# Kernel optimization log

Measured on AMD Instinct MI355X. Metric: run time of the kernel, lower is better.

## Reference

```python
import jax, jax.numpy as jnp
import numpy as np

NUM_STEPS = 5
RELAX = 1.5
EPS = 1e-5
SIZE = 128
OUT = 128
HSIZE = SIZE + OUT  # feature transformer width (256)


def bn_inf(x, g, b, m, v):
    # inference batch norm with running stats
    return g * (x - m) * jax.lax.rsqrt(v + EPS) + b


def glu(h):
    return h[:, :HSIZE] * jax.nn.sigmoid(h[:, HSIZE:])


def sparsemax(z):
    d = z.shape[-1]
    z_sorted = -jnp.sort(-z, axis=-1)  # descending
    z_cum = jnp.cumsum(z_sorted, axis=-1)
    k = jnp.arange(1, d + 1, dtype=z.dtype)
    support = 1.0 + k * z_sorted > z_cum
    k_z = jnp.sum(support, axis=-1, keepdims=True)  # int support size
    tau = (jnp.take_along_axis(z_cum, k_z - 1, axis=-1) - 1.0) / k_z.astype(z.dtype)
    return jnp.maximum(z - tau, 0.0)


def feat_transformer(x, Ws0, Ws1, Wu_t, g, b, m, v):
    # 4 GLU FeatureBlocks: blocks 0,1 use shared fc weights, 2,3 unshared
    sqrt_half = jnp.sqrt(jnp.asarray(0.5, x.dtype))
    h = glu(bn_inf(x @ Ws0, g[0], b[0], m[0], v[0]))
    h = h * sqrt_half + glu(bn_inf(h @ Ws1, g[1], b[1], m[1], v[1]))
    h = h * sqrt_half + glu(bn_inf(h @ Wu_t[0], g[2], b[2], m[2], v[2]))
    h = h * sqrt_half + glu(bn_inf(h @ Wu_t[1], g[3], b[3], m[3], v[3]))
    return h


def setup_inputs() -> dict:
    key = jax.random.key(0)
    ks = jax.random.split(key, 20)
    B, F = 32768, 512
    U = 2 * HSIZE  # GLU fc units = 512
    T = NUM_STEPS + 1
    sc = 0.05
    inp = {}
    inp['features'] = jax.random.normal(ks[0], (B, F), jnp.float32)
    inp['bn0_g'] = 1.0 + 0.1 * jax.random.normal(ks[1], (F,), jnp.float32)
    inp['bn0_b'] = 0.1 * jax.random.normal(ks[2], (F,), jnp.float32)
    inp['bn0_m'] = 0.1 * jax.random.normal(ks[3], (F,), jnp.float32)
    inp['bn0_v'] = jax.random.uniform(ks[4], (F,), jnp.float32, 0.5, 1.5)
    inp['Ws0'] = sc * jax.random.normal(ks[5], (F, U), jnp.float32)
    inp['Ws1'] = sc * jax.random.normal(ks[6], (HSIZE, U), jnp.float32)
    inp['Wu'] = sc * jax.random.normal(ks[7], (T, 2, HSIZE, U), jnp.float32)
    inp['ft_g'] = 1.0 + 0.1 * jax.random.normal(ks[8], (T, 4, U), jnp.float32)
    inp['ft_b'] = 0.1 * jax.random.normal(ks[9], (T, 4, U), jnp.float32)
    inp['ft_m'] = 0.1 * jax.random.normal(ks[10], (T, 4, U), jnp.float32)
    inp['ft_v'] = jax.random.uniform(ks[11], (T, 4, U), jnp.float32, 0.5, 1.5)
    inp['W_att'] = sc * jax.random.normal(ks[12], (NUM_STEPS, SIZE, F), jnp.float32)
    inp['att_g'] = 1.0 + 0.1 * jax.random.normal(ks[13], (NUM_STEPS, F), jnp.float32)
    inp['att_b'] = 0.1 * jax.random.normal(ks[14], (NUM_STEPS, F), jnp.float32)
    inp['att_m'] = 0.1 * jax.random.normal(ks[15], (NUM_STEPS, F), jnp.float32)
    inp['att_v'] = jax.random.uniform(ks[16], (NUM_STEPS, F), jnp.float32, 0.5, 1.5)
    inp['Wf'] = sc * jax.random.normal(ks[17], (SIZE, OUT), jnp.float32)
    inp['bf'] = jnp.zeros((OUT,), jnp.float32)
    return inp


def reference(features, bn0_g, bn0_b, bn0_m, bn0_v, Ws0, Ws1, Wu,
              ft_g, ft_b, ft_m, ft_v, W_att, att_g, att_b, att_m, att_v, Wf, bf):
    B = features.shape[0]
    feats = bn_inf(features, bn0_g, bn0_b, bn0_m, bn0_v)
    prior = jnp.ones_like(feats)
    out_acc = jnp.zeros((B, OUT), feats.dtype)
    x = feat_transformer(feats, Ws0, Ws1, Wu[0], ft_g[0], ft_b[0], ft_m[0], ft_v[0])
    masks = []
    for s in range(NUM_STEPS):
        att = bn_inf(x[:, OUT:] @ W_att[s], att_g[s], att_b[s], att_m[s], att_v[s])
        mask = sparsemax(att * prior)
        prior = prior * (RELAX - mask)
        masks.append(mask)
        x = feat_transformer(mask * feats, Ws0, Ws1, Wu[s + 1],
                             ft_g[s + 1], ft_b[s + 1], ft_m[s + 1], ft_v[s + 1])
        out_acc = out_acc + jax.nn.relu(x[:, :OUT])
    final = out_acc @ Wf + bf
    return final, jnp.stack(masks)
```

## Files before the change

### kernel.cpp

```cpp
#include <hip/hip_runtime.h>
#include <hip/hip_bf16.h>
#include <math.h>

#define B_ROWS   32768
#define NSTEPS   5
#define EPS_BN   1e-5f
#define RELAX_C  1.5f
#define SQRT_HALF 0.70710678118654752440f

typedef _Float16 f16;
typedef _Float16 f16x4 __attribute__((ext_vector_type(4)));
typedef _Float16 f16x8 __attribute__((ext_vector_type(8)));
typedef float    f32x4 __attribute__((ext_vector_type(4)));

__device__ __forceinline__ int glu_perm2(int c) {
    int g = c >> 5, o = c & 31;
    return (o < 16) ? (g * 16 + o) : (g * 16 + (o - 16) + 256);
}

__device__ __forceinline__ void gload16(const void* g, void* l) {
    __builtin_amdgcn_global_load_lds(
        (const __attribute__((address_space(1))) unsigned int*)g,
        (__attribute__((address_space(3))) unsigned int*)l, 16, 0, 0);
}

__global__ void prep_bn_kernel(
    const float* __restrict__ bn0_g, const float* __restrict__ bn0_b,
    const float* __restrict__ bn0_m, const float* __restrict__ bn0_v,
    const float* __restrict__ ft_g, const float* __restrict__ ft_b,
    const float* __restrict__ ft_m, const float* __restrict__ ft_v,
    const float* __restrict__ att_g, const float* __restrict__ att_b,
    const float* __restrict__ att_m, const float* __restrict__ att_v,
    float* __restrict__ sc0, float* __restrict__ sh0,
    float* __restrict__ ftS, float* __restrict__ ftH,
    float* __restrict__ attS, float* __restrict__ attH)
{
    int idx = blockIdx.x * blockDim.x + threadIdx.x;
    if (idx < 512) {
        float s = bn0_g[idx] * rsqrtf(bn0_v[idx] + EPS_BN);
        sc0[idx] = s;
        sh0[idx] = bn0_b[idx] - bn0_m[idx] * s;
    } else if (idx < 512 + 24 * 512) {
        int q = idx - 512;
        int tb = q >> 9;
        int c = q & 511;
        int src = tb * 512 + glu_perm2(c);
        float s = ft_g[src] * rsqrtf(ft_v[src] + EPS_BN);
        ftS[q] = s;
        ftH[q] = ft_b[src] - ft_m[src] * s;
    } else if (idx < 512 + 24 * 512 + 5 * 512) {
        int q = idx - 512 - 24 * 512;
        float s = att_g[q] * rsqrtf(att_v[q] + EPS_BN);
        attS[q] = s;
        attH[q] = att_b[q] - att_m[q] * s;
    }
}

__global__ void wprep_all(const float* __restrict__ Ws0, const float* __restrict__ Ws1,
                          const float* __restrict__ Wu,  const float* __restrict__ Wat,
                          f16* __restrict__ ws0, f16* __restrict__ ws1,
                          f16* __restrict__ wu,  f16* __restrict__ wat)
{
    int i = blockIdx.x * 256 + threadIdx.x;
    if (i < 262144) {
        int n = i >> 9, k = i & 511;
        ws0[i] = (f16)Ws0[(k << 9) + glu_perm2(n)];
    } else if (i < 393216) {
        int j = i - 262144;
        int n = j >> 8, k = j & 255;
        ws1[j] = (f16)Ws1[(k << 9) + glu_perm2(n)];
    } else if (i < 1966080) {
        int j = i - 393216;
        int mat = j >> 17;
        int r = j & 131071;
        int n = r >> 8, k = r & 255;
        wu[j] = (f16)Wu[(mat << 17) + (k << 9) + glu_perm2(n)];
    } else if (i < 2293760) {
        int j = i - 1966080;
        int mat = j >> 16;
        int r = j & 65535;
        int n = r >> 7, k = r & 127;
        wat[j] = (f16)Wat[(mat << 16) + (k << 9) + n];
    }
}

__global__ void bn0zero_kernel(const float* __restrict__ x,
                               const float* __restrict__ sc,
                               const float* __restrict__ sh,
                               f16* __restrict__ fh,
                               float* __restrict__ oacc)
{
    const int b = blockIdx.x;
    if (b < 16384) {
        int i = b * 256 + threadIdx.x;
        int base = i * 4;
        int c = base & 511;
        float4 xv = *(const float4*)(x + base);
        f16x4 hv;
        hv.x = (f16)(xv.x * sc[c]     + sh[c]);
        hv.y = (f16)(xv.y * sc[c + 1] + sh[c + 1]);
        hv.z = (f16)(xv.z * sc[c + 2] + sh[c + 2]);
        hv.w = (f16)(xv.w * sc[c + 3] + sh[c + 3]);
        *(f16x4*)(fh + base) = hv;
    } else {
        int i = (b - 16384) * 256 + threadIdx.x;
        ((float4*)oacc)[i] = make_float4(0.f, 0.f, 0.f, 0.f);
    }
}

template<int MODE, int NT>
__global__ __launch_bounds__(512, 4) void gemm_conveyor(
    const f16* __restrict__ A, const int ldA,
    const f16* __restrict__ B,
    const float* __restrict__ scale, const float* __restrict__ shift,
    const f16* __restrict__ res,
    f16* __restrict__ out,
    float* __restrict__ oacc)
{
    constexpr int K = NT * 32;
    __shared__ __align__(16) char smem[3 * 24576];
    const int tid  = threadIdx.x;
    const int lane = tid & 63;
    const int w    = tid >> 6;
    const int wm   = w >> 1;
    const int wn   = w & 1;
    const int lr   = lane & 15;
    const int lh   = lane >> 4;
    const int d    = blockIdx.x;
    const int bid  = (d & 7) * 64 + (d >> 3);
    const int row0 = (bid >> 2) * 256;
    const int bcol = (bid & 3) * 128;

    const int c0 = 3 * w, c1 = 3 * w + 1, c2 = 3 * w + 2;
    const bool a0 = c0 < 16, a1 = c1 < 16, a2 = c2 < 16;
    const char* p0 = a0 ? (const char*)(A + (size_t)(row0 + c0 * 16 + lr) * ldA + lh * 8)
                        : (const char*)(B + (size_t)(bcol + (c0 - 16) * 16 + lr) * K + lh * 8);
    const char* p1 = a1 ? (const char*)(A + (size_t)(row0 + c1 * 16 + lr) * ldA + lh * 8)
                        : (const char*)(B + (size_t)(bcol + (c1 - 16) * 16 + lr) * K + lh * 8);
    const char* p2 = a2 ? (const char*)(A + (size_t)(row0 + c2 * 16 + lr) * ldA + lh * 8)
                        : (const char*)(B + (size_t)(bcol + (c2 - 16) * 16 + lr) * K + lh * 8);
    const int d0 = c0 * 1024, d1 = c1 * 1024, d2 = c2 * 1024;

    f32x4 acc[4][4];
    #pragma unroll
    for (int m = 0; m < 4; ++m)
        #pragma unroll
        for (int n = 0; n < 4; ++n)
            acc[m][n] = f32x4{0.f, 0.f, 0.f, 0.f};

    auto STAGE = [&](int s) {
        const int ko = s * 64;
        char* ring = smem + (s % 3) * 24576;
        gload16(p0 + ko, ring + d0);
        gload16(p1 + ko, ring + d1);
        gload16(p2 + ko, ring + d2);
    };

    STAGE(0); STAGE(1);

    for (int s = 0; s < NT; ++s) {
        if (s + 1 < NT) asm volatile("s_waitcnt vmcnt(3)" ::: "memory");
        else            asm volatile("s_waitcnt vmcnt(0)" ::: "memory");
        __builtin_amdgcn_s_barrier();
        asm volatile("" ::: "memory");
        if (s + 2 < NT) STAGE(s + 2);

        const char* L = smem + (s % 3) * 24576;
        f16x8 a[4], b[4];
        #pragma unroll
        for (int m = 0; m < 4; ++m)
            a[m] = *(const f16x8*)(L + (wm * 4 + m) * 1024 + lane * 16);
        #pragma unroll
        for (int n = 0; n < 4; ++n)
            b[n] = *(const f16x8*)(L + 16384 + (wn * 4 + n) * 1024 + lane * 16);
        __builtin_amdgcn_s_setprio(1);
        #pragma unroll
        for (int n = 0; n < 4; ++n)
            #pragma unroll
            for (int m = 0; m < 4; ++m)
                acc[m][n] = __builtin_amdgcn_mfma_f32_16x16x32_f16(a[m], b[n], acc[m][n], 0, 0, 0);
        __builtin_amdgcn_s_setprio(0);
    }

    const int rbase = row0 + wm * 64;
    #pragma unroll
    for (int p = 0; p < 2; ++p) {
        const int cb = bcol + wn * 64 + p * 32;
        const float sA = scale[cb + lr],      hA = shift[cb + lr];
        const float sB = scale[cb + 16 + lr], hB = shift[cb + 16 + lr];
        const int oc = (cb >> 1) + lr;
        #pragma unroll
        for (int m = 0; m < 4; ++m) {
            #pragma unroll
            for (int r = 0; r < 4; ++r) {
                const int row = rbase + m * 16 + lh * 4 + r;
                float y0 = acc[m][2 * p][r]     * sA + hA;
                float y1 = acc[m][2 * p + 1][r] * sB + hB;
                float val = y0 / (1.f + expf(-y1));
                if constexpr (MODE >= 1)
                    val += SQRT_HALF * (float)res[(size_t)row * 256 + oc];
                if constexpr (MODE <= 1) {
                    out[(size_t)row * 256 + oc] = (f16)val;
                } else {
                    if (oc < 128) {
                        if (oacc) oacc[(size_t)row * 128 + oc] += fmaxf(val, 0.f);
                    } else {
                        out[(size_t)row * 128 + (oc - 128)] = (f16)val;
                    }
                }
            }
        }
    }
}

template<int USE_PRIOR>
__global__ __launch_bounds__(256, 2) void att_sparsemax_kernel(
    const f16* __restrict__ A,
    const f16* __restrict__ Bw,
    const float* __restrict__ scale, const float* __restrict__ shift,
    const f16* __restrict__ feats,
    f16* __restrict__ prior,
    float* __restrict__ mask_out,
    f16* __restrict__ mf)
{
    __shared__ float attLds[32 * 512];
    const int tid  = threadIdx.x;
    const int lane = tid & 63;
    const int w    = tid >> 6;
    const int brow = blockIdx.x * 32;
    const int lr   = lane & 15;
    const int lk   = (lane >> 4) * 8;

    f32x4 acc[2][8];
    #pragma unroll
    for (int m = 0; m < 2; ++m)
        #pragma unroll
        for (int n = 0; n < 8; ++n)
            acc[m][n] = f32x4{0.f, 0.f, 0.f, 0.f};

    const f16* pa = A + (size_t)(brow + lr) * 128 + lk;
    const f16* pb = Bw + (size_t)(w * 128 + lr) * 128 + lk;

    f16x8 a0[2], b0[8], a1[2], b1[8];
    #pragma unroll
    for (int m = 0; m < 2; ++m) a0[m] = *(const f16x8*)(pa + m * 16 * 128);
    #pragma unroll
    for (int n = 0; n < 8; ++n) b0[n] = *(const f16x8*)(pb + n * 16 * 128);

    #pragma unroll
    for (int t = 0; t < 4; t += 2) {
        #pragma unroll
        for (int m = 0; m < 2; ++m) a1[m] = *(const f16x8*)(pa + m * 16 * 128 + (t + 1) * 32);
        #pragma unroll
        for (int n = 0; n < 8; ++n) b1[n] = *(const f16x8*)(pb + n * 16 * 128 + (t + 1) * 32);
        #pragma unroll
        for (int n = 0; n < 8; ++n)
            #pragma unroll
            for (int m = 0; m < 2; ++m)
                acc[m][n] = __builtin_amdgcn_mfma_f32_16x16x32_f16(a0[m], b0[n], acc[m][n], 0, 0, 0);
        if (t + 2 < 4) {
            #pragma unroll
            for (int m = 0; m < 2; ++m) a0[m] = *(const f16x8*)(pa + m * 16 * 128 + (t + 2) * 32);
            #pragma unroll
            for (int n = 0; n < 8; ++n) b0[n] = *(const f16x8*)(pb + n * 16 * 128 + (t + 2) * 32);
        }
        #pragma unroll
        for (int n = 0; n < 8; ++n)
            #pragma unroll
            for (int m = 0; m < 2; ++m)
                acc[m][n] = __builtin_amdgcn_mfma_f32_16x16x32_f16(a1[m], b1[n], acc[m][n], 0, 0, 0);
    }

    #pragma unroll
    for (int m = 0; m < 2; ++m) {
        const int r0 = m * 16 + (lane >> 4) * 4;
        #pragma unroll
        for (int n = 0; n < 8; ++n) {
            const int col = w * 128 + n * 16 + lr;
            const float s = scale[col], h = shift[col];
            #pragma unroll
            for (int r = 0; r < 4; ++r)
                attLds[(r0 + r) * 512 + col] = acc[m][n][r] * s + h;
        }
    }
    __syncthreads();

    for (int rr = 0; rr < 8; ++rr) {
        const int row = w * 8 + rr;
        const int grow = brow + row;
        const size_t gbase = (size_t)grow * 512 + lane;

        float z[8], pr[8];
        #pragma unroll
        for (int j = 0; j < 8; ++j) {
            pr[j] = USE_PRIOR ? (float)prior[gbase + j * 64] : 1.0f;
            z[j] = attLds[row * 512 + lane + j * 64] * pr[j];
        }
        float mx = z[0];
        #pragma unroll
        for (int j = 1; j < 8; ++j) mx = fmaxf(mx, z[j]);
        #pragma unroll
        for (int off = 32; off; off >>= 1) mx = fmaxf(mx, __shfl_xor(mx, off));

        float tau = mx - 1.0f;
        for (int it = 0; it < 20; ++it) {
            float s = 0.f, c = 0.f;
            #pragma unroll
            for (int j = 0; j < 8; ++j) {
                float dz = z[j] - tau;
                if (dz > 0.f) { s += dz; c += 1.f; }
            }
            #pragma unroll
            for (int off = 32; off; off >>= 1) {
                s += __shfl_xor(s, off);
                c += __shfl_xor(c, off);
            }
            float tn = tau + (s - 1.0f) / c;
            if (!(tn > tau)) break;
            tau = tn;
        }

        #pragma unroll
        for (int j = 0; j < 8; ++j) {
            const size_t ix = gbase + j * 64;
            float m = fmaxf(z[j] - tau, 0.f);
            __builtin_nontemporal_store(m, &mask_out[ix]);
            prior[ix] = (f16)(pr[j] * (RELAX_C - m));
            mf[ix] = (f16)(m * (float)feats[ix]);
        }
    }
}

__global__ __launch_bounds__(256) void gemm_f32_final(
    const float* __restrict__ A,
    const float* __restrict__ W,
    const float* __restrict__ bias,
    float* __restrict__ out)
{
    __shared__ float As[16][128];
    __shared__ float Bs[16][128];
    const int tid = threadIdx.x;
    const int tm = tid >> 4, tn = tid & 15;
    const int brow = blockIdx.x * 128;
    float acc[8][8] = {};
    for (int k0 = 0; k0 < 128; k0 += 16) {
        #pragma unroll
        for (int i = 0; i < 2; ++i) {
            int f = tid + i * 256;
            int row = f >> 2, kq = (f & 3) << 2;
            float4 av = *(const float4*)(A + (size_t)(brow + row) * 128 + k0 + kq);
            As[kq + 0][row] = av.x;
            As[kq + 1][row] = av.y;
            As[kq + 2][row] = av.z;
            As[kq + 3][row] = av.w;
            int kr = f >> 5, nq = (f & 31) << 2;
            *(float4*)(&Bs[kr][nq]) = *(const float4*)(W + (size_t)(k0 + kr) * 128 + nq);
        }
        __syncthreads();
        #pragma unroll
        for (int kk = 0; kk < 16; ++kk) {
            float a[8], b[8];
            *(float4*)(a)     = *(const float4*)(&As[kk][tm * 8]);
            *(float4*)(a + 4) = *(const float4*)(&As[kk][tm * 8 + 4]);
            *(float4*)(b)     = *(const float4*)(&Bs[kk][tn * 8]);
            *(float4*)(b + 4) = *(const float4*)(&Bs[kk][tn * 8 + 4]);
            #pragma unroll
            for (int i = 0; i < 8; ++i)
                #pragma unroll
                for (int j = 0; j < 8; ++j)
                    acc[i][j] += a[i] * b[j];
        }
        __syncthreads();
    }
    #pragma unroll
    for (int i = 0; i < 8; ++i) {
        int row = brow + tm * 8 + i;
        #pragma unroll
        for (int j = 0; j < 8; ++j)
            out[(size_t)row * 128 + tn * 8 + j] = acc[i][j] + bias[tn * 8 + j];
    }
}

extern "C" void kernel_launch(void* const* d_in, const int* in_sizes, int n_in,
                              void* d_out, int out_size, void* d_ws, size_t ws_size,
                              hipStream_t stream)
{
    const float* features = (const float*)d_in[0];
    const float* bn0_g = (const float*)d_in[1];
    const float* bn0_b = (const float*)d_in[2];
    const float* bn0_m = (const float*)d_in[3];
    const float* bn0_v = (const float*)d_in[4];
    const float* Ws0   = (const float*)d_in[5];
    const float* Ws1   = (const float*)d_in[6];
    const float* Wu    = (const float*)d_in[7];
    const float* ft_g  = (const float*)d_in[8];
    const float* ft_b  = (const float*)d_in[9];
    const float* ft_m  = (const float*)d_in[10];
    const float* ft_v  = (const float*)d_in[11];
    const float* W_att = (const float*)d_in[12];
    const float* att_g = (const float*)d_in[13];
    const float* att_b = (const float*)d_in[14];
    const float* att_m = (const float*)d_in[15];
    const float* att_v = (const float*)d_in[16];
    const float* Wf    = (const float*)d_in[17];
    const float* bf    = (const float*)d_in[18];
    float* out = (float*)d_out;

    char* wp = (char*)d_ws;
    auto alloc = [&](size_t bytes) { char* r = wp; wp += (bytes + 255) & ~(size_t)255; return r; };
    const size_t BR = B_ROWS;
    f16* feats  = (f16*)alloc(BR * 512 * 2);
    f16* mfbuf  = (f16*)alloc(BR * 512 * 2);
    f16* ubuf   = (f16*)alloc(BR * 256 * 2);
    f16* vbuf   = (f16*)alloc(BR * 256 * 2);
    f16* xhalf  = (f16*)alloc(BR * 128 * 2);
    f16* prior  = (f16*)alloc(BR * 512 * 2);
    float* oacc  = (float*)alloc(BR * 128 * 4);
    f16* ws0  = (f16*)alloc(512 * 512 * 2);
    f16* ws1  = (f16*)alloc(512 * 256 * 2);
    f16* wu   = (f16*)alloc((size_t)12 * 512 * 256 * 2);
    f16* wat  = (f16*)alloc((size_t)5 * 512 * 128 * 2);
    float* ftS  = (float*)alloc(24 * 512 * 4);
    float* ftH  = (float*)alloc(24 * 512 * 4);
    float* attS = (float*)alloc(5 * 512 * 4);
    float* attH = (float*)alloc(5 * 512 * 4);
    float* sc0  = (float*)alloc(512 * 4);
    float* sh0  = (float*)alloc(512 * 4);

    prep_bn_kernel<<<60, 256, 0, stream>>>(
        bn0_g, bn0_b, bn0_m, bn0_v, ft_g, ft_b, ft_m, ft_v,
        att_g, att_b, att_m, att_v, sc0, sh0, ftS, ftH, attS, attH);
    wprep_all<<<8960, 256, 0, stream>>>(Ws0, Ws1, Wu, W_att, ws0, ws1, wu, wat);
    bn0zero_kernel<<<20480, 256, 0, stream>>>(features, sc0, sh0, feats, oacc);

    auto ft = [&](const f16* in, int t, bool accum) {
        const f16* wu0 = wu + (size_t)(t * 2 + 0) * 131072;
        const f16* wu1 = wu + (size_t)(t * 2 + 1) * 131072;
        gemm_conveyor<0, 16><<<512, 512, 0, stream>>>(in, 512, ws0,
            ftS + (t * 4 + 0) * 512, ftH + (t * 4 + 0) * 512,
            nullptr, ubuf, nullptr);
        gemm_conveyor<1, 8><<<512, 512, 0, stream>>>(ubuf, 256, ws1,
            ftS + (t * 4 + 1) * 512, ftH + (t * 4 + 1) * 512,
            ubuf, vbuf, nullptr);
        gemm_conveyor<1, 8><<<512, 512, 0, stream>>>(vbuf, 256, wu0,
            ftS + (t * 4 + 2) * 512, ftH + (t * 4 + 2) * 512,
            vbuf, ubuf, nullptr);
        gemm_conveyor<2, 8><<<512, 512, 0, stream>>>(ubuf, 256, wu1,
            ftS + (t * 4 + 3) * 512, ftH + (t * 4 + 3) * 512,
            ubuf, xhalf, accum ? oacc : nullptr);
    };

    ft(feats, 0, false);

    for (int s = 0; s < NSTEPS; ++s) {
        float* mask_s = out + 4194304 + (size_t)s * 16777216;
        if (s == 0)
            att_sparsemax_kernel<0><<<B_ROWS / 32, 256, 0, stream>>>(
                xhalf, wat + (size_t)s * 65536,
                attS + s * 512, attH + s * 512,
                feats, prior, mask_s, mfbuf);
        else
            att_sparsemax_kernel<1><<<B_ROWS / 32, 256, 0, stream>>>(
                xhalf, wat + (size_t)s * 65536,
                attS + s * 512, attH + s * 512,
                feats, prior, mask_s, mfbuf);
        ft(mfbuf, s + 1, true);
    }

    gemm_f32_final<<<B_ROWS / 128, 256, 0, stream>>>(oacc, Wf, bf, out);
}
```

Measured before the change: 1.047 ms.

## Shrink GEMM tiles to 128x128 with 4 waves and vectorize sparsemax row I/O

The fused GLU GEMM moves from 256x128 tiles with 8 waves to 128x128 tiles with 4 waves. Each wave now issues four async global-to-LDS loads per stage, the LDS ring shrinks, and twice as many blocks launch. The sparsemax epilogue switches to contiguous 8-element-per-lane access, so prior, feats, mask, prior-update and masked-feature I/O use vector loads and stores. The smaller tiles trade more B-operand reloads per row for more resident blocks, and the sparsemax change aims at fewer, wider memory transactions.

New measurement: 1.178 ms. +12.6%, slower.

```diff
diff --git a/kernel.cpp b/kernel.cpp
--- a/kernel.cpp
+++ b/kernel.cpp
@@ -109,7 +109,7 @@
 }
 
 template<int MODE, int NT>
-__global__ __launch_bounds__(512, 4) void gemm_conveyor(
+__global__ __launch_bounds__(256, 4) void gemm_mfma(
     const f16* __restrict__ A, const int ldA,
     const f16* __restrict__ B,
     const float* __restrict__ scale, const float* __restrict__ shift,
@@ -118,7 +118,7 @@
     float* __restrict__ oacc)
 {
     constexpr int K = NT * 32;
-    __shared__ __align__(16) char smem[3 * 24576];
+    __shared__ __align__(16) char smem[3 * 16384];
     const int tid  = threadIdx.x;
     const int lane = tid & 63;
     const int w    = tid >> 6;
@@ -127,19 +127,21 @@
     const int lr   = lane & 15;
     const int lh   = lane >> 4;
     const int d    = blockIdx.x;
-    const int bid  = (d & 7) * 64 + (d >> 3);
-    const int row0 = (bid >> 2) * 256;
+    const int bid  = (d & 7) * 128 + (d >> 3);
+    const int brow = (bid >> 2) * 128;
     const int bcol = (bid & 3) * 128;
 
-    const int c0 = 3 * w, c1 = 3 * w + 1, c2 = 3 * w + 2;
-    const bool a0 = c0 < 16, a1 = c1 < 16, a2 = c2 < 16;
-    const char* p0 = a0 ? (const char*)(A + (size_t)(row0 + c0 * 16 + lr) * ldA + lh * 8)
-                        : (const char*)(B + (size_t)(bcol + (c0 - 16) * 16 + lr) * K + lh * 8);
-    const char* p1 = a1 ? (const char*)(A + (size_t)(row0 + c1 * 16 + lr) * ldA + lh * 8)
-                        : (const char*)(B + (size_t)(bcol + (c1 - 16) * 16 + lr) * K + lh * 8);
-    const char* p2 = a2 ? (const char*)(A + (size_t)(row0 + c2 * 16 + lr) * ldA + lh * 8)
-                        : (const char*)(B + (size_t)(bcol + (c2 - 16) * 16 + lr) * K + lh * 8);
-    const int d0 = c0 * 1024, d1 = c1 * 1024, d2 = c2 * 1024;
+    const int c0 = 4 * w, c1 = 4 * w + 1, c2 = 4 * w + 2, c3 = 4 * w + 3;
+    const bool isA = (w < 2);
+    const char* p0 = isA ? (const char*)(A + (size_t)(brow + c0 * 16 + lr) * ldA + lh * 8)
+                         : (const char*)(B + (size_t)(bcol + (c0 - 8) * 16 + lr) * K + lh * 8);
+    const char* p1 = isA ? (const char*)(A + (size_t)(brow + c1 * 16 + lr) * ldA + lh * 8)
+                         : (const char*)(B + (size_t)(bcol + (c1 - 8) * 16 + lr) * K + lh * 8);
+    const char* p2 = isA ? (const char*)(A + (size_t)(brow + c2 * 16 + lr) * ldA + lh * 8)
+                         : (const char*)(B + (size_t)(bcol + (c2 - 8) * 16 + lr) * K + lh * 8);
+    const char* p3 = isA ? (const char*)(A + (size_t)(brow + c3 * 16 + lr) * ldA + lh * 8)
+                         : (const char*)(B + (size_t)(bcol + (c3 - 8) * 16 + lr) * K + lh * 8);
+    const int d0 = c0 * 1024, d1 = c1 * 1024, d2 = c2 * 1024, d3 = c3 * 1024;
 
     f32x4 acc[4][4];
     #pragma unroll
@@ -150,29 +152,30 @@
 
     auto STAGE = [&](int s) {
         const int ko = s * 64;
-        char* ring = smem + (s % 3) * 24576;
+        char* ring = smem + (s % 3) * 16384;
         gload16(p0 + ko, ring + d0);
         gload16(p1 + ko, ring + d1);
         gload16(p2 + ko, ring + d2);
+        gload16(p3 + ko, ring + d3);
     };
 
     STAGE(0); STAGE(1);
 
     for (int s = 0; s < NT; ++s) {
-        if (s + 1 < NT) asm volatile("s_waitcnt vmcnt(3)" ::: "memory");
+        if (s + 1 < NT) asm volatile("s_waitcnt vmcnt(4)" ::: "memory");
         else            asm volatile("s_waitcnt vmcnt(0)" ::: "memory");
         __builtin_amdgcn_s_barrier();
         asm volatile("" ::: "memory");
         if (s + 2 < NT) STAGE(s + 2);
 
-        const char* L = smem + (s % 3) * 24576;
+        const char* L = smem + (s % 3) * 16384;
         f16x8 a[4], b[4];
         #pragma unroll
         for (int m = 0; m < 4; ++m)
             a[m] = *(const f16x8*)(L + (wm * 4 + m) * 1024 + lane * 16);
         #pragma unroll
         for (int n = 0; n < 4; ++n)
-            b[n] = *(const f16x8*)(L + 16384 + (wn * 4 + n) * 1024 + lane * 16);
+            b[n] = *(const f16x8*)(L + 8192 + (wn * 4 + n) * 1024 + lane * 16);
         __builtin_amdgcn_s_setprio(1);
         #pragma unroll
         for (int n = 0; n < 4; ++n)
@@ -182,7 +185,7 @@
         __builtin_amdgcn_s_setprio(0);
     }
 
-    const int rbase = row0 + wm * 64;
+    const int rbase = brow + wm * 64;
     #pragma unroll
     for (int p = 0; p < 2; ++p) {
         const int cb = bcol + wn * 64 + p * 32;
@@ -285,16 +288,21 @@
     }
     __syncthreads();
 
+    const int cb8 = lane * 8;
     for (int rr = 0; rr < 8; ++rr) {
         const int row = w * 8 + rr;
         const int grow = brow + row;
-        const size_t gbase = (size_t)grow * 512 + lane;
+        const size_t g8 = (size_t)grow * 512 + cb8;
 
         float z[8], pr[8];
+        f16x8 prv;
+        if (USE_PRIOR) prv = *(const f16x8*)(prior + g8);
+        f32x4 za = *(const f32x4*)(&attLds[row * 512 + cb8]);
+        f32x4 zb = *(const f32x4*)(&attLds[row * 512 + cb8 + 4]);
         #pragma unroll
         for (int j = 0; j < 8; ++j) {
-            pr[j] = USE_PRIOR ? (float)prior[gbase + j * 64] : 1.0f;
-            z[j] = attLds[row * 512 + lane + j * 64] * pr[j];
+            pr[j] = USE_PRIOR ? (float)prv[j] : 1.0f;
+            z[j] = (j < 4 ? za[j] : zb[j - 4]) * pr[j];
         }
         float mx = z[0];
         #pragma unroll
@@ -320,14 +328,21 @@
             tau = tn;
         }
 
+        float mk[8];
+        f16x8 pnew, mfv;
+        f16x8 fv = *(const f16x8*)(feats + g8);
         #pragma unroll
         for (int j = 0; j < 8; ++j) {
-            const size_t ix = gbase + j * 64;
-            float m = fmaxf(z[j] - tau, 0.f);
-            __builtin_nontemporal_store(m, &mask_out[ix]);
-            prior[ix] = (f16)(pr[j] * (RELAX_C - m));
-            mf[ix] = (f16)(m * (float)feats[ix]);
-        }
+            mk[j] = fmaxf(z[j] - tau, 0.f);
+            pnew[j] = (f16)(pr[j] * (RELAX_C - mk[j]));
+            mfv[j] = (f16)(mk[j] * (float)fv[j]);
+        }
+        f32x4 m0 = {mk[0], mk[1], mk[2], mk[3]};
+        f32x4 m1 = {mk[4], mk[5], mk[6], mk[7]};
+        __builtin_nontemporal_store(m0, (f32x4*)(mask_out + g8));
+        __builtin_nontemporal_store(m1, (f32x4*)(mask_out + g8 + 4));
+        *(f16x8*)(prior + g8) = pnew;
+        *(f16x8*)(mf + g8) = mfv;
     }
 }
 
@@ -436,16 +451,16 @@
     auto ft = [&](const f16* in, int t, bool accum) {
         const f16* wu0 = wu + (size_t)(t * 2 + 0) * 131072;
         const f16* wu1 = wu + (size_t)(t * 2 + 1) * 131072;
-        gemm_conveyor<0, 16><<<512, 512, 0, stream>>>(in, 512, ws0,
+        gemm_mfma<0, 16><<<1024, 256, 0, stream>>>(in, 512, ws0,
             ftS + (t * 4 + 0) * 512, ftH + (t * 4 + 0) * 512,
             nullptr, ubuf, nullptr);
-        gemm_conveyor<1, 8><<<512, 512, 0, stream>>>(ubuf, 256, ws1,
+        gemm_mfma<1, 8><<<1024, 256, 0, stream>>>(ubuf, 256, ws1,
             ftS + (t * 4 + 1) * 512, ftH + (t * 4 + 1) * 512,
             ubuf, vbuf, nullptr);
-        gemm_conveyor<1, 8><<<512, 512, 0, stream>>>(vbuf, 256, wu0,
+        gemm_mfma<1, 8><<<1024, 256, 0, stream>>>(vbuf, 256, wu0,
             ftS + (t * 4 + 2) * 512, ftH + (t * 4 + 2) * 512,
             vbuf, ubuf, nullptr);
-        gemm_conveyor<2, 8><<<512, 512, 0, stream>>>(ubuf, 256, wu1,
+        gemm_mfma<2, 8><<<1024, 256, 0, stream>>>(ubuf, 256, wu1,
             ftS + (t * 4 + 3) * 512, ftH + (t * 4 + 3) * 512,
             ubuf, xhalf, accum ? oacc : nullptr);
     };
```

## Retile attention-sparsemax kernel to 64 rows with f16 LDS and vectorized I/O

Applied to the files above, without the earlier changes.

Each attention block now covers 64 rows with 8 waves, and each wave computes a 64x64 MFMA tile instead of 32x128. The goal is better reuse of the weight loads per block. The attention logits are staged in LDS as f16 instead of f32, which keeps LDS usage the same while doubling the rows held. Each lane now owns 8 contiguous columns, so prior, feats, mask, prior-update and masked-feature traffic use 16-byte vector loads and stores instead of strided scalar accesses. Rounding the logits to f16 before sparsemax adds a small precision loss that could change which entries end up in the support.

New measurement: 944.4 us. 9.8% less time.

```diff
diff --git a/kernel.cpp b/kernel.cpp
--- a/kernel.cpp
+++ b/kernel.cpp
@@ -214,7 +214,7 @@
 }
 
 template<int USE_PRIOR>
-__global__ __launch_bounds__(256, 2) void att_sparsemax_kernel(
+__global__ __launch_bounds__(512, 2) void att_sparsemax_kernel(
     const f16* __restrict__ A,
     const f16* __restrict__ Bw,
     const float* __restrict__ scale, const float* __restrict__ shift,
@@ -223,78 +223,66 @@
     float* __restrict__ mask_out,
     f16* __restrict__ mf)
 {
-    __shared__ float attLds[32 * 512];
+    __shared__ f16 attLds[64 * 512];
     const int tid  = threadIdx.x;
     const int lane = tid & 63;
     const int w    = tid >> 6;
-    const int brow = blockIdx.x * 32;
+    const int brow = blockIdx.x * 64;
     const int lr   = lane & 15;
     const int lk   = (lane >> 4) * 8;
 
-    f32x4 acc[2][8];
-    #pragma unroll
-    for (int m = 0; m < 2; ++m)
-        #pragma unroll
-        for (int n = 0; n < 8; ++n)
+    f32x4 acc[4][4];
+    #pragma unroll
+    for (int m = 0; m < 4; ++m)
+        #pragma unroll
+        for (int n = 0; n < 4; ++n)
             acc[m][n] = f32x4{0.f, 0.f, 0.f, 0.f};
 
     const f16* pa = A + (size_t)(brow + lr) * 128 + lk;
-    const f16* pb = Bw + (size_t)(w * 128 + lr) * 128 + lk;
-
-    f16x8 a0[2], b0[8], a1[2], b1[8];
-    #pragma unroll
-    for (int m = 0; m < 2; ++m) a0[m] = *(const f16x8*)(pa + m * 16 * 128);
-    #pragma unroll
-    for (int n = 0; n < 8; ++n) b0[n] = *(const f16x8*)(pb + n * 16 * 128);
-
-    #pragma unroll
-    for (int t = 0; t < 4; t += 2) {
-        #pragma unroll
-        for (int m = 0; m < 2; ++m) a1[m] = *(const f16x8*)(pa + m * 16 * 128 + (t + 1) * 32);
-        #pragma unroll
-        for (int n = 0; n < 8; ++n) b1[n] = *(const f16x8*)(pb + n * 16 * 128 + (t + 1) * 32);
-        #pragma unroll
-        for (int n = 0; n < 8; ++n)
-            #pragma unroll
-            for (int m = 0; m < 2; ++m)
-                acc[m][n] = __builtin_amdgcn_mfma_f32_16x16x32_f16(a0[m], b0[n], acc[m][n], 0, 0, 0);
-        if (t + 2 < 4) {
-            #pragma unroll
-            for (int m = 0; m < 2; ++m) a0[m] = *(const f16x8*)(pa + m * 16 * 128 + (t + 2) * 32);
-            #pragma unroll
-            for (int n = 0; n < 8; ++n) b0[n] = *(const f16x8*)(pb + n * 16 * 128 + (t + 2) * 32);
-        }
-        #pragma unroll
-        for (int n = 0; n < 8; ++n)
-            #pragma unroll
-            for (int m = 0; m < 2; ++m)
-                acc[m][n] = __builtin_amdgcn_mfma_f32_16x16x32_f16(a1[m], b1[n], acc[m][n], 0, 0, 0);
-    }
-
-    #pragma unroll
-    for (int m = 0; m < 2; ++m) {
-        const int r0 = m * 16 + (lane >> 4) * 4;
-        #pragma unroll
-        for (int n = 0; n < 8; ++n) {
-            const int col = w * 128 + n * 16 + lr;
-            const float s = scale[col], h = shift[col];
+    const f16* pb = Bw + (size_t)(w * 64 + lr) * 128 + lk;
+
+    #pragma unroll
+    for (int t = 0; t < 4; ++t) {
+        f16x8 a[4], b[4];
+        #pragma unroll
+        for (int m = 0; m < 4; ++m) a[m] = *(const f16x8*)(pa + m * 16 * 128 + t * 32);
+        #pragma unroll
+        for (int n = 0; n < 4; ++n) b[n] = *(const f16x8*)(pb + n * 16 * 128 + t * 32);
+        #pragma unroll
+        for (int n = 0; n < 4; ++n)
+            #pragma unroll
+            for (int m = 0; m < 4; ++m)
+                acc[m][n] = __builtin_amdgcn_mfma_f32_16x16x32_f16(a[m], b[n], acc[m][n], 0, 0, 0);
+    }
+
+    #pragma unroll
+    for (int n = 0; n < 4; ++n) {
+        const int col = w * 64 + n * 16 + lr;
+        const float s = scale[col], h = shift[col];
+        #pragma unroll
+        for (int m = 0; m < 4; ++m) {
+            const int r0 = m * 16 + (lane >> 4) * 4;
             #pragma unroll
             for (int r = 0; r < 4; ++r)
-                attLds[(r0 + r) * 512 + col] = acc[m][n][r] * s + h;
+                attLds[(r0 + r) * 512 + col] = (f16)(acc[m][n][r] * s + h);
         }
     }
     __syncthreads();
 
+    const int cb8 = lane * 8;
     for (int rr = 0; rr < 8; ++rr) {
         const int row = w * 8 + rr;
         const int grow = brow + row;
-        const size_t gbase = (size_t)grow * 512 + lane;
+        const size_t g8 = (size_t)grow * 512 + cb8;
 
         float z[8], pr[8];
+        f16x8 prv;
+        if (USE_PRIOR) prv = *(const f16x8*)(prior + g8);
+        f16x8 zv = *(const f16x8*)(&attLds[row * 512 + cb8]);
         #pragma unroll
         for (int j = 0; j < 8; ++j) {
-            pr[j] = USE_PRIOR ? (float)prior[gbase + j * 64] : 1.0f;
-            z[j] = attLds[row * 512 + lane + j * 64] * pr[j];
+            pr[j] = USE_PRIOR ? (float)prv[j] : 1.0f;
+            z[j] = (float)zv[j] * pr[j];
         }
         float mx = z[0];
         #pragma unroll
@@ -320,14 +308,21 @@
             tau = tn;
         }
 
+        float mk[8];
+        f16x8 pnew, mfv;
+        f16x8 fv = *(const f16x8*)(feats + g8);
         #pragma unroll
         for (int j = 0; j < 8; ++j) {
-            const size_t ix = gbase + j * 64;
-            float m = fmaxf(z[j] - tau, 0.f);
-            __builtin_nontemporal_store(m, &mask_out[ix]);
-            prior[ix] = (f16)(pr[j] * (RELAX_C - m));
-            mf[ix] = (f16)(m * (float)feats[ix]);
-        }
+            mk[j] = fmaxf(z[j] - tau, 0.f);
+            pnew[j] = (f16)(pr[j] * (RELAX_C - mk[j]));
+            mfv[j] = (f16)(mk[j] * (float)fv[j]);
+        }
+        f32x4 m0 = {mk[0], mk[1], mk[2], mk[3]};
+        f32x4 m1 = {mk[4], mk[5], mk[6], mk[7]};
+        __builtin_nontemporal_store(m0, (f32x4*)(mask_out + g8));
+        __builtin_nontemporal_store(m1, (f32x4*)(mask_out + g8 + 4));
+        *(f16x8*)(prior + g8) = pnew;
+        *(f16x8*)(mf + g8) = mfv;
     }
 }
 
@@ -455,12 +450,12 @@
     for (int s = 0; s < NSTEPS; ++s) {
         float* mask_s = out + 4194304 + (size_t)s * 16777216;
         if (s == 0)
-            att_sparsemax_kernel<0><<<B_ROWS / 32, 256, 0, stream>>>(
+            att_sparsemax_kernel<0><<<B_ROWS / 64, 512, 0, stream>>>(
                 xhalf, wat + (size_t)s * 65536,
                 attS + s * 512, attH + s * 512,
                 feats, prior, mask_s, mfbuf);
         else
-            att_sparsemax_kernel<1><<<B_ROWS / 32, 256, 0, stream>>>(
+            att_sparsemax_kernel<1><<<B_ROWS / 64, 512, 0, stream>>>(
                 xhalf, wat + (size_t)s * 65536,
                 attS + s * 512, attH + s * 512,
                 feats, prior, mask_s, mfbuf);
```
